# Optimization experiments

Measured on AMD Instinct MI355X. Metric: run time of the kernel, lower is better.

The kernel has to match this reference:

```python
import jax, jax.numpy as jnp
import numpy as np

DIM = 1024
NUM_HEADS = 16
HEAD_DIM = DIM // NUM_HEADS
B, T = 2, 2048


def setup_inputs() -> dict:
    key = jax.random.key(0)
    ks = jax.random.split(key, 7)
    x = jax.random.normal(ks[0], (B, T, DIM), dtype=jnp.float32)
    # causal mask, broadcastable over batch and heads
    mask = jnp.tril(jnp.ones((T, T), dtype=bool))[None, None, :, :]
    # rope tables for half rotary angles, tiled to head_dim (cat of two halves)
    pos = jnp.arange(T, dtype=jnp.float32)[:, None]
    inv_freq = 1.0 / (10000.0 ** (jnp.arange(0, HEAD_DIM, 2, dtype=jnp.float32) / HEAD_DIM))
    ang = pos * inv_freq[None, :]                      # [T, hd/2]
    ang = jnp.concatenate([ang, ang], axis=-1)         # [T, hd]
    rope_sin = jnp.sin(ang)[None, None, :, :]
    rope_cos = jnp.cos(ang)[None, None, :, :]
    s = 0.02
    qkv_w = jax.random.normal(ks[1], (DIM, 3 * DIM), dtype=jnp.float32) * s
    qkv_b = jnp.zeros((3 * DIM,), dtype=jnp.float32)
    proj_w = jax.random.normal(ks[2], (DIM, DIM), dtype=jnp.float32) * s
    proj_b = jnp.zeros((DIM,), dtype=jnp.float32)
    return {"x": x, "mask": mask, "rope_sin": rope_sin, "rope_cos": rope_cos,
            "qkv_w": qkv_w, "qkv_b": qkv_b, "proj_w": proj_w, "proj_b": proj_b}


def _rotate_half(t):
    half = t.shape[-1] // 2
    return jnp.concatenate([-t[..., half:], t[..., :half]], axis=-1)


def _apply_rope(t, sin, cos):
    return t * cos + _rotate_half(t) * sin


def reference(x, mask, rope_sin, rope_cos, qkv_w, qkv_b, proj_w, proj_b):
    Bb, Tt, C = x.shape
    qkv = x @ qkv_w + qkv_b                            # [B, T, 3C]
    q, k, v = jnp.split(qkv, 3, axis=-1)
    def split_heads(t):                                # [B, T, C] -> [B, H, T, hd]
        return t.reshape(Bb, Tt, NUM_HEADS, HEAD_DIM).transpose(0, 2, 1, 3)
    q, k, v = split_heads(q), split_heads(k), split_heads(v)
    sin = rope_sin[:, :, :Tt, :]
    cos = rope_cos[:, :, :Tt, :]
    q = _apply_rope(q, sin, cos)
    k = _apply_rope(k, sin, cos)
    att = jnp.einsum("bhqd,bhkd->bhqk", q, k) / (HEAD_DIM ** 0.5)
    att = jnp.where(mask, att, -jnp.inf)
    att = jax.nn.softmax(att, axis=-1)
    y = jnp.einsum("bhqk,bhkd->bhqd", att, v)          # [B, H, T, hd]
    y = y.transpose(0, 2, 1, 3).reshape(Bb, Tt, C)
    return y @ proj_w + proj_b
```

## Files before the change

### kernel.cpp

```cpp
#include <hip/hip_runtime.h>

typedef unsigned short u16;
typedef u16 u16x8 __attribute__((ext_vector_type(8)));
typedef __bf16 bf16x8 __attribute__((ext_vector_type(8)));
typedef float f32x4 __attribute__((ext_vector_type(4)));

#define T_SEQ 2048
#define DIM 1024
#define NH 16
#define HD 64

#define MFMA(a, b, c) __builtin_amdgcn_mfma_f32_16x16x32_bf16(a, b, c, 0, 0, 0)

__device__ __forceinline__ u16 f2bf(float f) {
  unsigned u = __builtin_bit_cast(unsigned, f);
  u = u + 0x7fffu + ((u >> 16) & 1u);
  return (u16)(u >> 16);
}

__device__ __forceinline__ bf16x8 ld8(const u16* p) {
  return __builtin_bit_cast(bf16x8, *(const u16x8*)p);
}

__device__ __forceinline__ void gload_lds16(const u16* g, u16* l) {
  __builtin_amdgcn_global_load_lds((const __attribute__((address_space(1))) void*)(g),
                                   (__attribute__((address_space(3))) void*)(l),
                                   16, 0, 0);
}

__global__ void k_prep(const float* __restrict__ X, u16* __restrict__ Y,
                       const float* __restrict__ Wq, u16* __restrict__ WqT,
                       const float* __restrict__ Wp, u16* __restrict__ WpT) {
  __shared__ float tile[32][33];
  int bid = blockIdx.x;
  if (bid < 4096) {
    int i = (bid * 256 + threadIdx.x) * 4;
    float4 f = *(const float4*)&X[i];
    ushort4 o = make_ushort4(f2bf(f.x), f2bf(f.y), f2bf(f.z), f2bf(f.w));
    *(ushort4*)&Y[i] = o;
    return;
  }
  const float* W; u16* WT; int K = 1024, N, bx, by;
  if (bid < 4096 + 3072) { int t = bid - 4096; W = Wq; WT = WqT; N = 3072; bx = t % 96; by = t / 96; }
  else                   { int t = bid - 7168; W = Wp; WT = WpT; N = 1024; bx = t % 32; by = t / 32; }
  int tx = threadIdx.x & 31, ty = threadIdx.x >> 5;
  int c0 = bx * 32, r0 = by * 32;
#pragma unroll
  for (int r = 0; r < 4; r++)
    tile[ty + r * 8][tx] = W[(r0 + ty + r * 8) * N + c0 + tx];
  __syncthreads();
#pragma unroll
  for (int r = 0; r < 4; r++)
    WT[(c0 + ty + r * 8) * K + r0 + tx] = f2bf(tile[tx][ty + r * 8]);
}


#define GEMM_CORE(Aptr, BTptr, Kdim, bxv, byv)                                    \
  const int tid = threadIdx.x;                                                    \
  const int lane = tid & 63, w = tid >> 6;                                        \
  const int l15 = lane & 15, quad = lane >> 4;                                    \
  const int wm = w >> 1, wn = w & 1;                                              \
  const int rowBase = (byv) * 128;                                                \
  const int colBase = (bxv) * 128;                                                \
  f32x4 acc[4][4];                                                                \
  _Pragma("unroll") for (int i = 0; i < 4; i++)                                   \
      _Pragma("unroll") for (int j = 0; j < 4; j++)                               \
          acc[i][j] = (f32x4){0.f, 0.f, 0.f, 0.f};                                \
  const int srow = lane >> 2;                 \
  const int schunk = (lane & 3) * 8;    \
  for (int k0 = 0; k0 < (Kdim); k0 += 32) {                                       \
    __syncthreads();                                                              \
    _Pragma("unroll") for (int p = 0; p < 2; p++) {                               \
      int rr = w * 32 + p * 16;                                                   \
      gload_lds16(&(Aptr)[(size_t)(rowBase + rr + srow) * (Kdim) + k0 + schunk],  \
                  &As[rr * 32]);                                                  \
      gload_lds16(&(BTptr)[(size_t)(colBase + rr + srow) * (Kdim) + k0 + schunk], \
                  &Bs[rr * 32]);                                                  \
    }                                                                             \
    __syncthreads();                 \
    bf16x8 af[4], bfv[4];                                                         \
    _Pragma("unroll") for (int i = 0; i < 4; i++) {                               \
      af[i] = ld8(&As[(wm * 64 + i * 16 + l15) * 32 + quad * 8]);                 \
      bfv[i] = ld8(&Bs[(wn * 64 + i * 16 + l15) * 32 + quad * 8]);                \
    }                                                                             \
    _Pragma("unroll") for (int i = 0; i < 4; i++)                                 \
        _Pragma("unroll") for (int j = 0; j < 4; j++)                             \
            acc[i][j] = MFMA(af[i], bfv[j], acc[i][j]);                           \
  }

__global__ __launch_bounds__(256) void k_gemm_qkv(
    const u16* __restrict__ A, const u16* __restrict__ BT,
    const float* __restrict__ bias,
    const float* __restrict__ rsin, const float* __restrict__ rcos,
    u16* __restrict__ qb, u16* __restrict__ kb, u16* __restrict__ vtb) {
  __shared__ __align__(16) u16 As[128 * 32];
  __shared__ __align__(16) u16 Bs[128 * 32];
  const int n = blockIdx.x, xcd = n & 7, s = n >> 3;
  const int cg = xcd & 1, rg = xcd >> 1;
  const int bxv = cg * 12 + (s >> 3);
  const int byv = rg * 8 + (s & 7);
  GEMM_CORE(A, BT, DIM, bxv, byv)

#pragma unroll
  for (int j = 0; j < 4; j++) {
    float bv = bias[colBase + wn * 64 + j * 16 + l15];
#pragma unroll
    for (int i = 0; i < 4; i++)
#pragma unroll
      for (int r = 0; r < 4; r++) acc[i][j][r] += bv;
  }

  const int colW = colBase + wn * 64;
  const int sec = colW >> 10;
  const int hh = (colW & 1023) >> 6;

#pragma unroll
  for (int i = 0; i < 4; i++) {
#pragma unroll
    for (int r = 0; r < 4; r++) {
      int grow = rowBase + wm * 64 + i * 16 + quad * 4 + r;
      int b = grow >> 11, t = grow & 2047;
#pragma unroll
      for (int j = 0; j < 4; j++) {
        int d = j * 16 + l15;
        float v = acc[i][j][r];
        if (sec == 2) {
          vtb[((b * NH + hh) * HD + d) * T_SEQ + t] = f2bf(v);
        } else {
          float pr = acc[i][j ^ 2][r];
          float rot = (j < 2) ? -pr : pr;
          float rv = v * rcos[t * HD + d] + rot * rsin[t * HD + d];
          if (sec == 0)
            qb[((b * NH + hh) * T_SEQ + t) * HD + d] = f2bf(rv * 0.125f);
          else
            kb[((b * NH + hh) * T_SEQ + t) * HD + d] = f2bf(rv);
        }
      }
    }
  }
}

__global__ __launch_bounds__(256) void k_gemm_proj(
    const u16* __restrict__ A, const u16* __restrict__ BT,
    const float* __restrict__ bias, float* __restrict__ C) {
  __shared__ __align__(16) u16 As[128 * 32];
  __shared__ __align__(16) u16 Bs[128 * 32];
  const int n = blockIdx.x, xcd = n & 7, s = n >> 3;
  const int cg = xcd & 1, rg = xcd >> 1;
  const int bxv = cg * 4 + (s >> 3);
  const int byv = rg * 8 + (s & 7);
  GEMM_CORE(A, BT, DIM, bxv, byv)

#pragma unroll
  for (int i = 0; i < 4; i++)
#pragma unroll
    for (int r = 0; r < 4; r++) {
      int grow = rowBase + wm * 64 + i * 16 + quad * 4 + r;
#pragma unroll
      for (int j = 0; j < 4; j++) {
        int col = colBase + wn * 64 + j * 16 + l15;
        C[grow * DIM + col] = acc[i][j][r] + bias[col];
      }
    }
}

#define KLD 72
#define VLD 136

__global__ __launch_bounds__(256) void k_attn(
    const u16* __restrict__ qb, const u16* __restrict__ kb,
    const u16* __restrict__ vtb, u16* __restrict__ yb) {
  __shared__ __align__(16) u16 Qs[64 * KLD];
  __shared__ __align__(16) u16 Ks[128 * KLD];
  __shared__ __align__(16) u16 VTs[64 * VLD];
  __shared__ __align__(16) u16 Ps[4][16 * VLD];
  const int tid = threadIdx.x;
  const int lane = tid & 63, w = tid >> 6;
  const int l15 = lane & 15, quad = lane >> 4;
  const int bh = blockIdx.x;
  const int qt = 31 - blockIdx.y;

  const u16* qp = qb + (size_t)bh * T_SEQ * HD;
  const u16* kp = kb + (size_t)bh * T_SEQ * HD;
  const u16* vp = vtb + (size_t)bh * HD * T_SEQ;

  {
    int sr = tid >> 3, sc = (tid & 7) * 8;
#pragma unroll
    for (int p = 0; p < 2; p++) {
      int r = sr + p * 32;
      *(u16x8*)&Qs[r * KLD + sc] = *(const u16x8*)&qp[(qt * 64 + r) * HD + sc];
    }
  }
  __syncthreads();
  bf16x8 qa0 = ld8(&Qs[(w * 16 + l15) * KLD + quad * 8]);
  bf16x8 qa1 = ld8(&Qs[(w * 16 + l15) * KLD + 32 + quad * 8]);

  f32x4 o[4];
#pragma unroll
  for (int j = 0; j < 4; j++) o[j] = (f32x4){0.f, 0.f, 0.f, 0.f};
  float li[4] = {0.f, 0.f, 0.f, 0.f};

  const int nch = (qt + 2) >> 1;
  const int qrow_base = qt * 64 + w * 16 + quad * 4;

  for (int c = 0; c < nch; c++) {
    {
      int sr = tid >> 3, sc = (tid & 7) * 8;
#pragma unroll
      for (int p = 0; p < 4; p++) {
        int r = sr + p * 32;
        *(u16x8*)&Ks[r * KLD + sc] = *(const u16x8*)&kp[(c * 128 + r) * HD + sc];
      }
      int vr = tid >> 4, vc = (tid & 15) * 8;
#pragma unroll
      for (int p = 0; p < 4; p++) {
        int r = vr + p * 16;
        *(u16x8*)&VTs[r * VLD + vc] = *(const u16x8*)&vp[r * T_SEQ + c * 128 + vc];
      }
    }
    __syncthreads();

    f32x4 s[8];
#pragma unroll
    for (int j = 0; j < 8; j++) {
      s[j] = (f32x4){0.f, 0.f, 0.f, 0.f};
      bf16x8 b0 = ld8(&Ks[(j * 16 + l15) * KLD + quad * 8]);
      bf16x8 b1 = ld8(&Ks[(j * 16 + l15) * KLD + 32 + quad * 8]);
      s[j] = MFMA(qa0, b0, s[j]);
      s[j] = MFMA(qa1, b1, s[j]);
    }

    u16* ps = &Ps[w][0];
    const bool lastc = (c == nch - 1);
#pragma unroll
    for (int r = 0; r < 4; r++) {
#pragma unroll
      for (int j = 0; j < 8; j++) {
        float e = __expf(s[j][r]);
        if (lastc && (c * 128 + j * 16 + l15 > qrow_base + r)) e = 0.f;
        li[r] += e;
        ps[(quad * 4 + r) * VLD + j * 16 + l15] = f2bf(e);
      }
    }

#pragma unroll
    for (int c4 = 0; c4 < 4; c4++) {
      bf16x8 pa = ld8(&ps[l15 * VLD + c4 * 32 + quad * 8]);
#pragma unroll
      for (int j2 = 0; j2 < 4; j2++) {
        bf16x8 vb = ld8(&VTs[(j2 * 16 + l15) * VLD + c4 * 32 + quad * 8]);
        o[j2] = MFMA(pa, vb, o[j2]);
      }
    }
    __syncthreads();
  }

#pragma unroll
  for (int r = 0; r < 4; r++) {
#pragma unroll
    for (int off = 8; off >= 1; off >>= 1) li[r] += __shfl_xor(li[r], off, 16);
    li[r] = 1.0f / li[r];
  }

  const int b = bh >> 4, h = bh & 15;
#pragma unroll
  for (int j = 0; j < 4; j++)
#pragma unroll
    for (int r = 0; r < 4; r++) {
      int t = qt * 64 + w * 16 + quad * 4 + r;
      int d = j * 16 + l15;
      yb[((b * T_SEQ + t) * NH + h) * HD + d] = f2bf(o[j][r] * li[r]);
    }
}

extern "C" void kernel_launch(void* const* d_in, const int* in_sizes, int n_in,
                              void* d_out, int out_size, void* d_ws, size_t ws_size,
                              hipStream_t stream) {
  const float* x      = (const float*)d_in[0];
  const float* rsin   = (const float*)d_in[2];
  const float* rcos   = (const float*)d_in[3];
  const float* qkv_w  = (const float*)d_in[4];
  const float* qkv_b  = (const float*)d_in[5];
  const float* proj_w = (const float*)d_in[6];
  const float* proj_b = (const float*)d_in[7];
  float* out = (float*)d_out;

  char* ws = (char*)d_ws;
  u16* x_bf  = (u16*)(ws);
  u16* qkvT  = (u16*)(ws + (8ull << 20));
  u16* projT = (u16*)(ws + (14ull << 20));
  u16* q_buf = (u16*)(ws + (16ull << 20));
  u16* k_buf = (u16*)(ws + (24ull << 20));
  u16* vT    = (u16*)(ws + (32ull << 20));
  u16* y_buf = (u16*)(ws + (40ull << 20));

  hipLaunchKernelGGL(k_prep, dim3(8192), dim3(256), 0, stream,
                     x, x_bf, qkv_w, qkvT, proj_w, projT);
  hipLaunchKernelGGL(k_gemm_qkv, dim3(768), dim3(256), 0, stream,
                     x_bf, qkvT, qkv_b, rsin, rcos, q_buf, k_buf, vT);
  hipLaunchKernelGGL(k_attn, dim3(32, 32), dim3(256), 0, stream,
                     q_buf, k_buf, vT, y_buf);
  hipLaunchKernelGGL(k_gemm_proj, dim3(256), dim3(256), 0, stream,
                     y_buf, projT, proj_b, out);
}
```

Baseline: 217.8 us.

## Double-buffer LDS tiles in GEMM core to overlap loads with MFMA

The shared GEMM core used by the QKV and projection kernels now keeps two LDS buffers for the A and B tiles. The loop is unrolled by two k-steps, so the async global-to-LDS load of the next tile is issued before the MFMAs on the current tile run. This hides global load latency behind compute and cuts the barriers per k-step from two to one. In exchange, LDS use per block doubles to 32 KB, which could lower occupancy.

```diff
diff --git a/kernel.cpp b/kernel.cpp
--- a/kernel.cpp
+++ b/kernel.cpp
@@ -55,6 +55,29 @@
 }
 
 
+#define GEMM_STAGE(buf, kk)                                                       \
+  {                                                                               \
+    _Pragma("unroll") for (int p = 0; p < 2; p++) {                               \
+      int rr = w * 32 + p * 16;                                                   \
+      gload_lds16(&Agp[(size_t)(rowBase + rr + srow) * Kd + (kk) + schunk],       \
+                  &As[buf][rr * 32]);                                             \
+      gload_lds16(&Bgp[(size_t)(colBase + rr + srow) * Kd + (kk) + schunk],       \
+                  &Bs[buf][rr * 32]);                                             \
+    }                                                                             \
+  }
+
+#define GEMM_COMPUTE(buf)                                                         \
+  {                                                                               \
+    bf16x8 af[4], bfv[4];                                                         \
+    _Pragma("unroll") for (int i = 0; i < 4; i++) {                               \
+      af[i] = ld8(&As[buf][(wm * 64 + i * 16 + l15) * 32 + quad * 8]);            \
+      bfv[i] = ld8(&Bs[buf][(wn * 64 + i * 16 + l15) * 32 + quad * 8]);           \
+    }                                                                             \
+    _Pragma("unroll") for (int i = 0; i < 4; i++)                                 \
+        _Pragma("unroll") for (int j = 0; j < 4; j++)                             \
+            acc[i][j] = MFMA(af[i], bfv[j], acc[i][j]);                           \
+  }
+
 #define GEMM_CORE(Aptr, BTptr, Kdim, bxv, byv)                                    \
   const int tid = threadIdx.x;                                                    \
   const int lane = tid & 63, w = tid >> 6;                                        \
@@ -62,30 +85,26 @@
   const int wm = w >> 1, wn = w & 1;                                              \
   const int rowBase = (byv) * 128;                                                \
   const int colBase = (bxv) * 128;                                                \
+  const u16* Agp = (Aptr);                                                        \
+  const u16* Bgp = (BTptr);                                                       \
+  const int Kd = (Kdim);                                                          \
   f32x4 acc[4][4];                                                                \
   _Pragma("unroll") for (int i = 0; i < 4; i++)                                   \
       _Pragma("unroll") for (int j = 0; j < 4; j++)                               \
           acc[i][j] = (f32x4){0.f, 0.f, 0.f, 0.f};                                \
   const int srow = lane >> 2;                 \
   const int schunk = (lane & 3) * 8;    \
-  for (int k0 = 0; k0 < (Kdim); k0 += 32) {                                       \
-    __syncthreads();                                                              \
-    _Pragma("unroll") for (int p = 0; p < 2; p++) {                               \
-      int rr = w * 32 + p * 16;                                                   \
-      gload_lds16(&(Aptr)[(size_t)(rowBase + rr + srow) * (Kdim) + k0 + schunk],  \
-                  &As[rr * 32]);                                                  \
-      gload_lds16(&(BTptr)[(size_t)(colBase + rr + srow) * (Kdim) + k0 + schunk], \
-                  &Bs[rr * 32]);                                                  \
-    }                                                                             \
-    __syncthreads();                 \
-    bf16x8 af[4], bfv[4];                                                         \
-    _Pragma("unroll") for (int i = 0; i < 4; i++) {                               \
-      af[i] = ld8(&As[(wm * 64 + i * 16 + l15) * 32 + quad * 8]);                 \
-      bfv[i] = ld8(&Bs[(wn * 64 + i * 16 + l15) * 32 + quad * 8]);                \
-    }                                                                             \
-    _Pragma("unroll") for (int i = 0; i < 4; i++)                                 \
-        _Pragma("unroll") for (int j = 0; j < 4; j++)                             \
-            acc[i][j] = MFMA(af[i], bfv[j], acc[i][j]);                           \
+  GEMM_STAGE(0, 0)                                                                \
+  __syncthreads();                                    \
+    \
+    \
+  for (int k0 = 0; k0 < Kd; k0 += 64) {                                          \
+    if (k0 + 32 < Kd) GEMM_STAGE(1, k0 + 32)              \
+    GEMM_COMPUTE(0)                                       \
+    __syncthreads();             \
+    if (k0 + 64 < Kd) GEMM_STAGE(0, k0 + 64)              \
+    GEMM_COMPUTE(1)                                       \
+    __syncthreads();                                                             \
   }
 
 __global__ __launch_bounds__(256) void k_gemm_qkv(
@@ -93,8 +112,8 @@
     const float* __restrict__ bias,
     const float* __restrict__ rsin, const float* __restrict__ rcos,
     u16* __restrict__ qb, u16* __restrict__ kb, u16* __restrict__ vtb) {
-  __shared__ __align__(16) u16 As[128 * 32];
-  __shared__ __align__(16) u16 Bs[128 * 32];
+  __shared__ __align__(16) u16 As[2][128 * 32];
+  __shared__ __align__(16) u16 Bs[2][128 * 32];
   const int n = blockIdx.x, xcd = n & 7, s = n >> 3;
   const int cg = xcd & 1, rg = xcd >> 1;
   const int bxv = cg * 12 + (s >> 3);
@@ -143,8 +162,8 @@
 __global__ __launch_bounds__(256) void k_gemm_proj(
     const u16* __restrict__ A, const u16* __restrict__ BT,
     const float* __restrict__ bias, float* __restrict__ C) {
-  __shared__ __align__(16) u16 As[128 * 32];
-  __shared__ __align__(16) u16 Bs[128 * 32];
+  __shared__ __align__(16) u16 As[2][128 * 32];
+  __shared__ __align__(16) u16 Bs[2][128 * 32];
   const int n = blockIdx.x, xcd = n & 7, s = n >> 3;
   const int cg = xcd & 1, rg = xcd >> 1;
   const int bxv = cg * 4 + (s >> 3);
```

Measured after the change: 221.4 us. Within noise of the previous version (+1.7%).
